# Kernel tuning notes

Hardware: AMD Instinct MI355X
Metric: run time of the kernel (lower is better)

Reference implementation:

```python
import jax, jax.numpy as jnp
import numpy as np

N_NODES = 100000
N_EDGES = 1600000
N_FEAT = 128
N_CLASSES = 10
N_GRAPHS = 256


def setup_inputs() -> dict:
    key = jax.random.key(0)
    ks = jax.random.split(key, 16)
    x = jax.random.normal(ks[0], (N_NODES, N_FEAT), dtype=jnp.float32)
    edge_index = jax.random.randint(ks[1], (2, N_EDGES), 0, N_NODES, dtype=jnp.int64)
    batch = jnp.sort(jax.random.randint(ks[2], (N_NODES,), 0, N_GRAPHS, dtype=jnp.int64))
    s = 0.1
    # GAT1: in=128 -> heads=8, out_per_head=8, concat -> 64
    W1 = jax.random.normal(ks[3], (N_FEAT, 64), dtype=jnp.float32) * s
    a_src1 = jax.random.normal(ks[4], (8, 8), dtype=jnp.float32) * s
    a_dst1 = jax.random.normal(ks[5], (8, 8), dtype=jnp.float32) * s
    b1 = jnp.zeros((64,), jnp.float32)
    # GAT2: in=64 -> heads=1, out=128
    W2 = jax.random.normal(ks[6], (64, 128), dtype=jnp.float32) * s
    a_src2 = jax.random.normal(ks[7], (1, 128), dtype=jnp.float32) * s
    a_dst2 = jax.random.normal(ks[8], (1, 128), dtype=jnp.float32) * s
    b2 = jnp.zeros((128,), jnp.float32)
    fc_w = jax.random.normal(ks[9], (128, N_CLASSES), dtype=jnp.float32) * s
    fc_b = jnp.zeros((N_CLASSES,), jnp.float32)
    return {"x": x, "edge_index": edge_index, "batch": batch,
            "W1": W1, "a_src1": a_src1, "a_dst1": a_dst1, "b1": b1,
            "W2": W2, "a_src2": a_src2, "a_dst2": a_dst2, "b2": b2,
            "fc_w": fc_w, "fc_b": fc_b}


def _segment_softmax(e, seg, n):
    # e: [E, H]; softmax over edges sharing the same destination node
    m = jax.ops.segment_max(e, seg, num_segments=n)
    m = jnp.where(jnp.isfinite(m), m, jnp.zeros_like(m))  # guard isolated nodes
    ex = jnp.exp(e - m[seg])
    s = jax.ops.segment_sum(ex, seg, num_segments=n)
    return ex / (s[seg] + jnp.asarray(1e-16, e.dtype))


def _gat_conv(x, src, dst, W, a_src, a_dst, bias):
    # PyG GATConv (eval mode, self-loops already appended to src/dst)
    H, C = a_src.shape
    n = x.shape[0]
    h = (x @ W).reshape(n, H, C)                      # [N,H,C]
    al_s = jnp.einsum('nhc,hc->nh', h, a_src)          # [N,H]
    al_d = jnp.einsum('nhc,hc->nh', h, a_dst)
    e = jax.nn.leaky_relu(al_s[src] + al_d[dst], 0.2)  # [E,H]
    alpha = _segment_softmax(e, dst, n)                # [E,H]
    out = jax.ops.segment_sum(h[src] * alpha[..., None], dst, num_segments=n)  # [N,H,C]
    return out.reshape(n, H * C) + bias                # concat=True (H=1 layer2 is identity reshape)


def reference(x, edge_index, batch, W1, a_src1, a_dst1, b1, W2, a_src2, a_dst2, b2, fc_w, fc_b):
    n = x.shape[0]
    loop = jnp.arange(n, dtype=edge_index.dtype)
    src = jnp.concatenate([edge_index[0], loop])       # add self-loops (PyG default)
    dst = jnp.concatenate([edge_index[1], loop])
    x1 = jax.nn.relu(_gat_conv(x, src, dst, W1, a_src1, a_dst1, b1))
    # dropout p=0.6 is identity in eval mode
    x2 = _gat_conv(x1, src, dst, W2, a_src2, a_dst2, b2)
    cnt = jax.ops.segment_sum(jnp.ones((n,), x2.dtype), batch, num_segments=N_GRAPHS)
    pooled = jax.ops.segment_sum(x2, batch, num_segments=N_GRAPHS) / jnp.maximum(cnt, 1.0)[:, None]
    logits = pooled @ fc_w + fc_b
    return jax.nn.log_softmax(logits, axis=1)
```

## Files before the change

### kernel.cpp

```cpp
#include <hip/hip_runtime.h>
#include <math.h>

typedef unsigned int uint;
typedef unsigned short ushort;
typedef unsigned char uchar;
typedef __attribute__((ext_vector_type(2))) float v2f;

#define S1 4.0f
#define S2 16.0f

template <bool HI>
__device__ inline v2f fp8x2f(uint u) {
    return __builtin_amdgcn_cvt_pk_f32_fp8((int)u, HI);
}

__global__ __launch_bounds__(256) void k_gemm1(const float* __restrict__ x,
                                               const float* __restrict__ W1,
                                               const float* __restrict__ as1,
                                               const float* __restrict__ ad1,
                                               uchar* __restrict__ h1f8,
                                               float* __restrict__ al1s,
                                               float* __restrict__ al1d, int N) {
    __shared__ float sB[128 * 64];
    __shared__ float sA[64 * 68];
    const int t = threadIdx.x;
    const int n0 = blockIdx.x * 64;
    {
        const float4* w4 = (const float4*)W1;
        float4* s4 = (float4*)sB;
#pragma unroll
        for (int i = 0; i < 8; ++i) s4[t + i * 256] = w4[t + i * 256];
    }
    const int r0 = (t >> 3) * 2;
    const int c0 = (t & 7) * 8;
    float acc0[8] = {0, 0, 0, 0, 0, 0, 0, 0};
    float acc1[8] = {0, 0, 0, 0, 0, 0, 0, 0};
    for (int kb = 0; kb < 2; ++kb) {
        __syncthreads();
#pragma unroll
        for (int i = 0; i < 4; ++i) {
            int idx = t + i * 256;
            int r = idx >> 4, kc = idx & 15;
            int n = n0 + r;
            float4 v = make_float4(0.f, 0.f, 0.f, 0.f);
            if (n < N) v = ((const float4*)x)[(size_t)n * 32 + kb * 16 + kc];
            *(float4*)&sA[r * 68 + kc * 4] = v;
        }
        __syncthreads();
        const float* bptr = &sB[kb * 64 * 64];
#pragma unroll 8
        for (int kk = 0; kk < 64; ++kk) {
            float a0 = sA[r0 * 68 + kk];
            float a1 = sA[(r0 + 1) * 68 + kk];
            const float* bp = &bptr[kk * 64 + c0];
            float4 b0 = *(const float4*)bp;
            float4 b1v = *(const float4*)(bp + 4);
            acc0[0] += a0 * b0.x; acc0[1] += a0 * b0.y; acc0[2] += a0 * b0.z; acc0[3] += a0 * b0.w;
            acc0[4] += a0 * b1v.x; acc0[5] += a0 * b1v.y; acc0[6] += a0 * b1v.z; acc0[7] += a0 * b1v.w;
            acc1[0] += a1 * b0.x; acc1[1] += a1 * b0.y; acc1[2] += a1 * b0.z; acc1[3] += a1 * b0.w;
            acc1[4] += a1 * b1v.x; acc1[5] += a1 * b1v.y; acc1[6] += a1 * b1v.z; acc1[7] += a1 * b1v.w;
        }
    }
    float ps0 = 0.f, pd0 = 0.f, ps1 = 0.f, pd1 = 0.f;
#pragma unroll
    for (int i = 0; i < 8; ++i) {
        float ws = as1[c0 + i], wd = ad1[c0 + i];
        ps0 += acc0[i] * ws; pd0 += acc0[i] * wd;
        ps1 += acc1[i] * ws; pd1 += acc1[i] * wd;
    }
    int n = n0 + r0;
    int head = t & 7;
    if (n < N) {
        int q0 = 0, q1 = 0;
        q0 = __builtin_amdgcn_cvt_pk_fp8_f32(acc0[0] * S1, acc0[1] * S1, q0, false);
        q0 = __builtin_amdgcn_cvt_pk_fp8_f32(acc0[2] * S1, acc0[3] * S1, q0, true);
        q1 = __builtin_amdgcn_cvt_pk_fp8_f32(acc0[4] * S1, acc0[5] * S1, q1, false);
        q1 = __builtin_amdgcn_cvt_pk_fp8_f32(acc0[6] * S1, acc0[7] * S1, q1, true);
        uint2 p; p.x = (uint)q0; p.y = (uint)q1;
        *(uint2*)&h1f8[(size_t)n * 64 + c0] = p;
        al1s[(size_t)n * 8 + head] = ps0;
        al1d[(size_t)n * 8 + head] = pd0;
    }
    if (n + 1 < N) {
        int q0 = 0, q1 = 0;
        q0 = __builtin_amdgcn_cvt_pk_fp8_f32(acc1[0] * S1, acc1[1] * S1, q0, false);
        q0 = __builtin_amdgcn_cvt_pk_fp8_f32(acc1[2] * S1, acc1[3] * S1, q0, true);
        q1 = __builtin_amdgcn_cvt_pk_fp8_f32(acc1[4] * S1, acc1[5] * S1, q1, false);
        q1 = __builtin_amdgcn_cvt_pk_fp8_f32(acc1[6] * S1, acc1[7] * S1, q1, true);
        uint2 p; p.x = (uint)q0; p.y = (uint)q1;
        *(uint2*)&h1f8[(size_t)(n + 1) * 64 + c0] = p;
        al1s[(size_t)(n + 1) * 8 + head] = ps1;
        al1d[(size_t)(n + 1) * 8 + head] = pd1;
    }
}

__global__ __launch_bounds__(256) void k_gemm2(const float* __restrict__ x1pre,
                                               const float* __restrict__ W2,
                                               const float* __restrict__ b1,
                                               const float* __restrict__ as2,
                                               const float* __restrict__ ad2,
                                               uchar* __restrict__ h2f8,
                                               float* __restrict__ al2s,
                                               float* __restrict__ al2d, int N) {
    __shared__ float sB[64 * 128];
    __shared__ float sA[64 * 68];
    const int t = threadIdx.x;
    const int n0 = blockIdx.x * 64;
    {
        const float4* w4 = (const float4*)W2;
        float4* s4 = (float4*)sB;
#pragma unroll
        for (int i = 0; i < 8; ++i) s4[t + i * 256] = w4[t + i * 256];
    }
#pragma unroll
    for (int i = 0; i < 4; ++i) {
        int idx = t + i * 256;
        int r = idx >> 4, kc = idx & 15;
        int n = n0 + r;
        float4 v = make_float4(0.f, 0.f, 0.f, 0.f);
        if (n < N) {
            v = ((const float4*)x1pre)[(size_t)n * 16 + kc];
            float4 bb = ((const float4*)b1)[kc];
            v.x = fmaxf(v.x + bb.x, 0.f);
            v.y = fmaxf(v.y + bb.y, 0.f);
            v.z = fmaxf(v.z + bb.z, 0.f);
            v.w = fmaxf(v.w + bb.w, 0.f);
        }
        *(float4*)&sA[r * 68 + kc * 4] = v;
    }
    __syncthreads();
    const int r0 = (t >> 3) * 2;
    const int cb = (t & 7) * 4;
    float acc0[16], acc1[16];
#pragma unroll
    for (int i = 0; i < 16; ++i) { acc0[i] = 0.f; acc1[i] = 0.f; }
#pragma unroll 4
    for (int k = 0; k < 64; ++k) {
        float a0 = sA[r0 * 68 + k];
        float a1 = sA[(r0 + 1) * 68 + k];
#pragma unroll
        for (int j = 0; j < 4; ++j) {
            float4 b = *(const float4*)&sB[k * 128 + cb + 32 * j];
            acc0[j * 4 + 0] += a0 * b.x; acc0[j * 4 + 1] += a0 * b.y;
            acc0[j * 4 + 2] += a0 * b.z; acc0[j * 4 + 3] += a0 * b.w;
            acc1[j * 4 + 0] += a1 * b.x; acc1[j * 4 + 1] += a1 * b.y;
            acc1[j * 4 + 2] += a1 * b.z; acc1[j * 4 + 3] += a1 * b.w;
        }
    }
    float ps0 = 0.f, pd0 = 0.f, ps1 = 0.f, pd1 = 0.f;
#pragma unroll
    for (int j = 0; j < 4; ++j)
#pragma unroll
        for (int i = 0; i < 4; ++i) {
            int cc = cb + 32 * j + i;
            float ws = as2[cc], wd = ad2[cc];
            ps0 += acc0[j * 4 + i] * ws; pd0 += acc0[j * 4 + i] * wd;
            ps1 += acc1[j * 4 + i] * ws; pd1 += acc1[j * 4 + i] * wd;
        }
#pragma unroll
    for (int off = 1; off < 8; off <<= 1) {
        ps0 += __shfl_xor(ps0, off); pd0 += __shfl_xor(pd0, off);
        ps1 += __shfl_xor(ps1, off); pd1 += __shfl_xor(pd1, off);
    }
    int n = n0 + r0;
    if (n < N) {
#pragma unroll
        for (int j = 0; j < 4; ++j) {
            int q = 0;
            q = __builtin_amdgcn_cvt_pk_fp8_f32(acc0[j * 4 + 0] * S2, acc0[j * 4 + 1] * S2, q, false);
            q = __builtin_amdgcn_cvt_pk_fp8_f32(acc0[j * 4 + 2] * S2, acc0[j * 4 + 3] * S2, q, true);
            *(uint*)&h2f8[(size_t)n * 128 + cb + 32 * j] = (uint)q;
        }
        if ((t & 7) == 0) { al2s[n] = ps0; al2d[n] = pd0; }
    }
    if (n + 1 < N) {
#pragma unroll
        for (int j = 0; j < 4; ++j) {
            int q = 0;
            q = __builtin_amdgcn_cvt_pk_fp8_f32(acc1[j * 4 + 0] * S2, acc1[j * 4 + 1] * S2, q, false);
            q = __builtin_amdgcn_cvt_pk_fp8_f32(acc1[j * 4 + 2] * S2, acc1[j * 4 + 3] * S2, q, true);
            *(uint*)&h2f8[(size_t)(n + 1) * 128 + cb + 32 * j] = (uint)q;
        }
        if ((t & 7) == 0) { al2s[n + 1] = ps1; al2d[n + 1] = pd1; }
    }
}


__global__ __launch_bounds__(256) void k_hist(const int* __restrict__ dst,
                                              int* __restrict__ counts,
                                              int E, int CH, int NB) {
    __shared__ int hist[784];
    int t = threadIdx.x, b = blockIdx.x;
    for (int k = t; k < NB; k += 256) hist[k] = 0;
    __syncthreads();
    int e0 = b * CH;
    int e1 = e0 + CH; if (e1 > E) e1 = E;
    for (int e = e0 + t; e < e1; e += 256)
        atomicAdd(&hist[dst[e] >> 7], 1);
    __syncthreads();
    for (int k = t; k < NB; k += 256) counts[(size_t)b * NB + k] = hist[k];
}

__global__ __launch_bounds__(256) void k_bscan(int* __restrict__ counts,
                                               int* __restrict__ btot,
                                               int C, int NB) {
    __shared__ int sh[256];
    int t = threadIdx.x, k = blockIdx.x;
    int v[4];
#pragma unroll
    for (int i = 0; i < 4; ++i) {
        int b = t * 4 + i;
        v[i] = (b < C) ? counts[(size_t)b * NB + k] : 0;
    }
    int s = v[0] + v[1] + v[2] + v[3];
    sh[t] = s;
    __syncthreads();
    int accv = s;
    for (int off = 1; off < 256; off <<= 1) {
        int u = (t >= off) ? sh[t - off] : 0;
        __syncthreads();
        accv += u;
        sh[t] = accv;
        __syncthreads();
    }
    int excl = accv - s;
#pragma unroll
    for (int i = 0; i < 4; ++i) {
        int b = t * 4 + i;
        if (b < C) counts[(size_t)b * NB + k] = excl;
        excl += v[i];
    }
    if (t == 255) btot[k] = accv;
}

__global__ void k_bscan2(const int* __restrict__ btot, int* __restrict__ bbase,
                         int NB, int E) {
    __shared__ int sh[1024];
    int t = threadIdx.x;
    int v = (t < NB) ? btot[t] : 0;
    sh[t] = v;
    __syncthreads();
    int accv = v;
    for (int off = 1; off < 1024; off <<= 1) {
        int u = (t >= off) ? sh[t - off] : 0;
        __syncthreads();
        accv += u;
        sh[t] = accv;
        __syncthreads();
    }
    if (t < NB) bbase[t] = accv - v;
    if (t == 0) bbase[NB] = E;
}

__global__ __launch_bounds__(256) void k_bucket(const int* __restrict__ src,
                                                const int* __restrict__ dst,
                                                const int* __restrict__ counts,
                                                const int* __restrict__ bbase,
                                                int* __restrict__ ebuf,
                                                int E, int CH, int NB) {
    __shared__ int pos[784];
    int t = threadIdx.x, b = blockIdx.x;
    for (int k = t; k < NB; k += 256)
        pos[k] = bbase[k] + counts[(size_t)b * NB + k];
    __syncthreads();
    int e0 = b * CH;
    int e1 = e0 + CH; if (e1 > E) e1 = E;
    for (int e = e0 + t; e < e1; e += 256) {
        int d = dst[e], s = src[e];
        int p = atomicAdd(&pos[d >> 7], 1);
        ebuf[p] = (int)((uint)s | ((uint)(d & 127) << 25));
    }
}

__global__ __launch_bounds__(256) void k_csr(const int* __restrict__ bbase,
                                             const int* __restrict__ ebuf,
                                             int* __restrict__ row_ptr,
                                             int* __restrict__ col,
                                             int N, int E) {
    __shared__ int cnt[128];
    __shared__ int fill[128];
    __shared__ int rowb[128];
    __shared__ int sh[256];
    int t = threadIdx.x, k = blockIdx.x;
    int lo = bbase[k], hi = bbase[k + 1];
    int nlo = k << 7;
    int nn = N - nlo; if (nn > 128) nn = 128;
    if (t < 128) { cnt[t] = 0; fill[t] = 0; }
    __syncthreads();
    for (int i = lo + t; i < hi; i += 256)
        atomicAdd(&cnt[((uint)ebuf[i]) >> 25], 1);
    __syncthreads();
    int v = (t < nn) ? (cnt[t] + 1) : 0;
    sh[t] = v;
    __syncthreads();
    int accv = v;
    for (int off = 1; off < 256; off <<= 1) {
        int u = (t >= off) ? sh[t - off] : 0;
        __syncthreads();
        accv += u;
        sh[t] = accv;
        __syncthreads();
    }
    int fbase = lo + nlo;
    if (t < nn) {
        int rb = fbase + accv - v;
        rowb[t] = rb;
        row_ptr[nlo + t] = rb;
        col[rb + cnt[t]] = nlo + t;
    }
    if (k == 0 && t == 0) row_ptr[N] = E + N;
    __syncthreads();
    for (int i = lo + t; i < hi; i += 256) {
        uint e = (uint)ebuf[i];
        int j = (int)(e >> 25);
        int r = atomicAdd(&fill[j], 1);
        col[rowb[j] + r] = (int)(e & 0x1FFFFFFu);
    }
}

__global__ __launch_bounds__(256) void k_edge1(const uchar* __restrict__ h1f8,
                                               const float* __restrict__ al1s,
                                               const float* __restrict__ al1d,
                                               const int* __restrict__ row_ptr,
                                               const int* __restrict__ col,
                                               float* __restrict__ x1pre, int N) {
    int node = blockIdx.x * 4 + (threadIdx.x >> 6);
    if (node >= N) return;
    const int lane = threadIdx.x & 63;
    const int e8 = lane >> 3;
    const int h = lane & 7;
    const int g = lane >> 4;
    const int k4 = lane & 15;
    const int hh = k4 >> 1;
    const uint co = (uint)(k4 * 4);
    float a_d = al1d[(((uint)node) << 3) | (uint)h];
    const int s0 = row_ptr[node], s1 = row_ptr[node + 1];
    float den_part = 0.f;
    v2f accL = {0.f, 0.f};
    v2f accH = {0.f, 0.f};
    for (int base = s0; base < s1; base += 64) {
        int idx = base + lane;
        int cidx = idx < s1 ? idx : s1 - 1;
        int my_col = col[cidx];
        int cnt = s1 - base; if (cnt > 64) cnt = 64;
        int cntR = (cnt + 3) & ~3;
        int i = 0;
        for (; i + 16 <= cntR; i += 16) {
            int cA = __shfl(my_col, i + g);
            int cB = __shfl(my_col, i + 4 + g);
            int cC = __shfl(my_col, i + 8 + g);
            int cD = __shfl(my_col, i + 12 + g);
            uint hA = *(const uint*)(h1f8 + ((((uint)cA) << 6) | co));
            uint hB = *(const uint*)(h1f8 + ((((uint)cB) << 6) | co));
            uint hC = *(const uint*)(h1f8 + ((((uint)cC) << 6) | co));
            uint hD = *(const uint*)(h1f8 + ((((uint)cD) << 6) | co));
            int c0 = __shfl(my_col, i + e8);
            int c1 = __shfl(my_col, i + 8 + e8);
            float e0v = *(al1s + ((((uint)c0) << 3) | (uint)h)) + a_d;
            float e1v = *(al1s + ((((uint)c1) << 3) | (uint)h)) + a_d;
            e0v = e0v > 0.f ? e0v : 0.2f * e0v;
            e1v = e1v > 0.f ? e1v : 0.2f * e1v;
            float w0 = (base + i + e8 < s1) ? __expf(e0v) : 0.f;
            float w1 = (base + i + 8 + e8 < s1) ? __expf(e1v) : 0.f;
            den_part += w0 + w1;
            float wA = __shfl(w0, g * 8 + hh);
            float wB = __shfl(w0, (4 + g) * 8 + hh);
            float wC = __shfl(w1, g * 8 + hh);
            float wD = __shfl(w1, (4 + g) * 8 + hh);
            v2f wA2 = {wA, wA}, wB2 = {wB, wB}, wC2 = {wC, wC}, wD2 = {wD, wD};
            accL += wA2 * fp8x2f<false>(hA);
            accH += wA2 * fp8x2f<true>(hA);
            accL += wB2 * fp8x2f<false>(hB);
            accH += wB2 * fp8x2f<true>(hB);
            accL += wC2 * fp8x2f<false>(hC);
            accH += wC2 * fp8x2f<true>(hC);
            accL += wD2 * fp8x2f<false>(hD);
            accH += wD2 * fp8x2f<true>(hD);
        }
        int rem = cntR - i;
        if (rem & 8) {
            int cA = __shfl(my_col, i + g);
            int cB = __shfl(my_col, i + 4 + g);
            uint hA = *(const uint*)(h1f8 + ((((uint)cA) << 6) | co));
            uint hB = *(const uint*)(h1f8 + ((((uint)cB) << 6) | co));
            int c0 = __shfl(my_col, i + e8);
            float e0v = *(al1s + ((((uint)c0) << 3) | (uint)h)) + a_d;
            e0v = e0v > 0.f ? e0v : 0.2f * e0v;
            float w0 = (base + i + e8 < s1) ? __expf(e0v) : 0.f;
            den_part += w0;
            float wA = __shfl(w0, g * 8 + hh);
            float wB = __shfl(w0, (4 + g) * 8 + hh);
            v2f wA2 = {wA, wA}, wB2 = {wB, wB};
            accL += wA2 * fp8x2f<false>(hA);
            accH += wA2 * fp8x2f<true>(hA);
            accL += wB2 * fp8x2f<false>(hB);
            accH += wB2 * fp8x2f<true>(hB);
            i += 8;
        }
        if (rem & 4) {
            int cA = __shfl(my_col, i + g);
            uint hA = *(const uint*)(h1f8 + ((((uint)cA) << 6) | co));
            int c0 = __shfl(my_col, i + e8);
            float e0v = *(al1s + ((((uint)c0) << 3) | (uint)h)) + a_d;
            e0v = e0v > 0.f ? e0v : 0.2f * e0v;
            float w0 = (base + i + e8 < s1) ? __expf(e0v) : 0.f;
            den_part += w0;
            float wA = __shfl(w0, g * 8 + hh);
            v2f wA2 = {wA, wA};
            accL += wA2 * fp8x2f<false>(hA);
            accH += wA2 * fp8x2f<true>(hA);
        }
    }
    float a0 = accL.x, a1 = accL.y, a2 = accH.x, a3 = accH.y;
    a0 += __shfl_xor(a0, 16); a0 += __shfl_xor(a0, 32);
    a1 += __shfl_xor(a1, 16); a1 += __shfl_xor(a1, 32);
    a2 += __shfl_xor(a2, 16); a2 += __shfl_xor(a2, 32);
    a3 += __shfl_xor(a3, 16); a3 += __shfl_xor(a3, 32);
    den_part += __shfl_xor(den_part, 8);
    den_part += __shfl_xor(den_part, 16);
    den_part += __shfl_xor(den_part, 32);
    float den = __shfl(den_part, hh);
    if (lane < 16) {
        float invd = 1.f / (den * S1);
        ((float4*)x1pre)[(size_t)node * 16 + k4] =
            make_float4(a0 * invd, a1 * invd, a2 * invd, a3 * invd);
    }
}

__global__ __launch_bounds__(256) void k_edge2(const uchar* __restrict__ h2f8,
                                               const float* __restrict__ al2s,
                                               const float* __restrict__ al2d,
                                               const int* __restrict__ row_ptr,
                                               const int* __restrict__ col,
                                               const float* __restrict__ b2,
                                               float* __restrict__ x2, int N) {
    int node = blockIdx.x * 4 + (threadIdx.x >> 6);
    if (node >= N) return;
    const int lane = threadIdx.x & 63;
    const int g = lane >> 4;
    const int k8 = lane & 15;
    const uint co = (uint)(k8 * 8);
    float a_d = al2d[node];
    int s0 = row_ptr[node], s1 = row_ptr[node + 1];
    v2f acc0 = {0.f, 0.f}, acc1 = {0.f, 0.f}, acc2 = {0.f, 0.f}, acc3 = {0.f, 0.f};
    float den = 0.f;
    for (int base = s0; base < s1; base += 64) {
        int idx = base + lane;
        int cidx = idx < s1 ? idx : s1 - 1;
        int my_col = col[cidx];
        float my_e = *(al2s + (uint)my_col) + a_d;
        my_e = my_e > 0.f ? my_e : 0.2f * my_e;
        float my_w = (idx < s1) ? __expf(my_e) : 0.f;
        den += my_w;
        int cnt = s1 - base; if (cnt > 64) cnt = 64;
        int cntR = (cnt + 3) & ~3;
        int i = 0;
        for (; i + 16 <= cntR; i += 16) {
            int eA = i + g, eB = i + 4 + g, eC = i + 8 + g, eD = i + 12 + g;
            int cA = __shfl(my_col, eA), cB = __shfl(my_col, eB);
            int cC = __shfl(my_col, eC), cD = __shfl(my_col, eD);
            float wA = __shfl(my_w, eA), wB = __shfl(my_w, eB);
            float wC = __shfl(my_w, eC), wD = __shfl(my_w, eD);
            uint2 hA = *(const uint2*)(h2f8 + ((((uint)cA) << 7) | co));
            uint2 hB = *(const uint2*)(h2f8 + ((((uint)cB) << 7) | co));
            uint2 hC = *(const uint2*)(h2f8 + ((((uint)cC) << 7) | co));
            uint2 hD = *(const uint2*)(h2f8 + ((((uint)cD) << 7) | co));
            v2f wA2 = {wA, wA}, wB2 = {wB, wB}, wC2 = {wC, wC}, wD2 = {wD, wD};
            acc0 += wA2 * fp8x2f<false>(hA.x);
            acc1 += wA2 * fp8x2f<true>(hA.x);
            acc2 += wA2 * fp8x2f<false>(hA.y);
            acc3 += wA2 * fp8x2f<true>(hA.y);
            acc0 += wB2 * fp8x2f<false>(hB.x);
            acc1 += wB2 * fp8x2f<true>(hB.x);
            acc2 += wB2 * fp8x2f<false>(hB.y);
            acc3 += wB2 * fp8x2f<true>(hB.y);
            acc0 += wC2 * fp8x2f<false>(hC.x);
            acc1 += wC2 * fp8x2f<true>(hC.x);
            acc2 += wC2 * fp8x2f<false>(hC.y);
            acc3 += wC2 * fp8x2f<true>(hC.y);
            acc0 += wD2 * fp8x2f<false>(hD.x);
            acc1 += wD2 * fp8x2f<true>(hD.x);
            acc2 += wD2 * fp8x2f<false>(hD.y);
            acc3 += wD2 * fp8x2f<true>(hD.y);
        }
        int rem = cntR - i;
        if (rem & 8) {
            int eA = i + g, eB = i + 4 + g;
            int cA = __shfl(my_col, eA), cB = __shfl(my_col, eB);
            float wA = __shfl(my_w, eA), wB = __shfl(my_w, eB);
            uint2 hA = *(const uint2*)(h2f8 + ((((uint)cA) << 7) | co));
            uint2 hB = *(const uint2*)(h2f8 + ((((uint)cB) << 7) | co));
            v2f wA2 = {wA, wA}, wB2 = {wB, wB};
            acc0 += wA2 * fp8x2f<false>(hA.x);
            acc1 += wA2 * fp8x2f<true>(hA.x);
            acc2 += wA2 * fp8x2f<false>(hA.y);
            acc3 += wA2 * fp8x2f<true>(hA.y);
            acc0 += wB2 * fp8x2f<false>(hB.x);
            acc1 += wB2 * fp8x2f<true>(hB.x);
            acc2 += wB2 * fp8x2f<false>(hB.y);
            acc3 += wB2 * fp8x2f<true>(hB.y);
            i += 8;
        }
        if (rem & 4) {
            int eA = i + g;
            int cA = __shfl(my_col, eA);
            float wA = __shfl(my_w, eA);
            uint2 hA = *(const uint2*)(h2f8 + ((((uint)cA) << 7) | co));
            v2f wA2 = {wA, wA};
            acc0 += wA2 * fp8x2f<false>(hA.x);
            acc1 += wA2 * fp8x2f<true>(hA.x);
            acc2 += wA2 * fp8x2f<false>(hA.y);
            acc3 += wA2 * fp8x2f<true>(hA.y);
        }
    }
#pragma unroll
    for (int off = 1; off < 64; off <<= 1) den += __shfl_xor(den, off);
    float r0 = acc0.x, r1 = acc0.y, r2 = acc1.x, r3 = acc1.y;
    float r4 = acc2.x, r5 = acc2.y, r6 = acc3.x, r7 = acc3.y;
    r0 += __shfl_xor(r0, 16); r0 += __shfl_xor(r0, 32);
    r1 += __shfl_xor(r1, 16); r1 += __shfl_xor(r1, 32);
    r2 += __shfl_xor(r2, 16); r2 += __shfl_xor(r2, 32);
    r3 += __shfl_xor(r3, 16); r3 += __shfl_xor(r3, 32);
    r4 += __shfl_xor(r4, 16); r4 += __shfl_xor(r4, 32);
    r5 += __shfl_xor(r5, 16); r5 += __shfl_xor(r5, 32);
    r6 += __shfl_xor(r6, 16); r6 += __shfl_xor(r6, 32);
    r7 += __shfl_xor(r7, 16); r7 += __shfl_xor(r7, 32);
    if (lane < 16) {
        float invd = 1.f / (den * S2);
        const float4* bb = (const float4*)b2;
        float4 o0 = bb[k8 * 2], o1 = bb[k8 * 2 + 1];
        float4* dst = (float4*)(x2 + (size_t)node * 128 + k8 * 8);
        dst[0] = make_float4(r0 * invd + o0.x, r1 * invd + o0.y,
                             r2 * invd + o0.z, r3 * invd + o0.w);
        dst[1] = make_float4(r4 * invd + o1.x, r5 * invd + o1.y,
                             r6 * invd + o1.z, r7 * invd + o1.w);
    }
}

__global__ __launch_bounds__(128) void k_pool(const float* __restrict__ x2,
                                              const int* __restrict__ batch,
                                              float* __restrict__ pooled,
                                              float* __restrict__ cnt, int N) {
    int t = threadIdx.x;
    int nstart = blockIdx.x * 128;
    if (nstart >= N) return;
    int nend = nstart + 128;
    if (nend > N) nend = N;
    float acc = 0.f;
    int cur = batch[nstart];
    int count = 0;
    for (int n = nstart; n < nend; ++n) {
        int g = batch[n];
        if (g != cur) {
            atomicAdd(&pooled[(size_t)cur * 128 + t], acc);
            if (t == 0) atomicAdd(&cnt[cur], (float)count);
            acc = 0.f;
            count = 0;
            cur = g;
        }
        acc += x2[(size_t)n * 128 + t];
        ++count;
    }
    atomicAdd(&pooled[(size_t)cur * 128 + t], acc);
    if (t == 0) atomicAdd(&cnt[cur], (float)count);
}

__global__ __launch_bounds__(64) void k_fc(const float* __restrict__ pooled,
                                           const float* __restrict__ cnt,
                                           const float* __restrict__ fcw,
                                           const float* __restrict__ fcb,
                                           float* __restrict__ out, int G) {
    int g = blockIdx.x;
    int c = threadIdx.x;
    float2 p = ((const float2*)pooled)[(size_t)g * 64 + c];
    float inv = 1.f / fmaxf(cnt[g], 1.f);
    p.x *= inv; p.y *= inv;
    float l[10];
#pragma unroll
    for (int j = 0; j < 10; ++j)
        l[j] = p.x * fcw[(2 * c) * 10 + j] + p.y * fcw[(2 * c + 1) * 10 + j];
#pragma unroll
    for (int j = 0; j < 10; ++j)
        for (int off = 1; off < 64; off <<= 1) l[j] += __shfl_xor(l[j], off);
    if (c == 0) {
        float lj[10];
        float m = -1e30f;
#pragma unroll
        for (int j = 0; j < 10; ++j) {
            lj[j] = l[j] + fcb[j];
            m = fmaxf(m, lj[j]);
        }
        float s = 0.f;
#pragma unroll
        for (int j = 0; j < 10; ++j) s += expf(lj[j] - m);
        float ls = logf(s);
#pragma unroll
        for (int j = 0; j < 10; ++j) out[(size_t)g * 10 + j] = lj[j] - m - ls;
    }
}

extern "C" void kernel_launch(void* const* d_in, const int* in_sizes, int n_in,
                              void* d_out, int out_size, void* d_ws, size_t ws_size,
                              hipStream_t stream) {
    const float* x     = (const float*)d_in[0];
    const int*   ei    = (const int*)d_in[1];
    const int*   batch = (const int*)d_in[2];
    const float* W1    = (const float*)d_in[3];
    const float* as1   = (const float*)d_in[4];
    const float* ad1   = (const float*)d_in[5];
    const float* b1    = (const float*)d_in[6];
    const float* W2    = (const float*)d_in[7];
    const float* as2   = (const float*)d_in[8];
    const float* ad2   = (const float*)d_in[9];
    const float* b2    = (const float*)d_in[10];
    const float* fcw   = (const float*)d_in[11];
    const float* fcb   = (const float*)d_in[12];
    float* out = (float*)d_out;

    const int N = in_sizes[0] / 128;
    const int E = in_sizes[1] / 2;
    const int G = out_size / 10;
    const int* srcp = ei;
    const int* dstp = ei + E;

    float* wf = (float*)d_ws;
    uchar* h1f8   = (uchar*)wf;
    float* x1pre  = wf + (size_t)N * 16;
    float* x2     = wf;
    uchar* h2f8   = (uchar*)(wf + (size_t)N * 128);
    float* al1s_  = wf + (size_t)N * 160;
    float* al1d_  = wf + (size_t)N * 168;
    float* al2s_  = wf + (size_t)N * 176;
    float* al2d_  = wf + (size_t)N * 177;
    float* pooled = wf + (size_t)N * 178;
    float* cnt    = pooled + (size_t)G * 128;

    const int NB = (N + 127) >> 7;
    const int C  = 1024;
    const int CH = (E + C - 1) / C;

    int* ib = (int*)(((uintptr_t)(cnt + G) + 15) & ~(uintptr_t)15);
    int* ebuf    = ib;
    int* counts  = ib + (size_t)E;
    int* btot    = counts + (size_t)C * NB;
    int* bbase   = btot + NB;
    int* row_ptr = bbase + NB + 1;
    int* col     = row_ptr + N + 1;

    size_t zbytes = ((size_t)G * 128 + G) * sizeof(float);
    (void)hipMemsetAsync(pooled, 0, zbytes, stream);

    const int nb64 = (N + 63) / 64;
    const int nb4  = (N + 3) / 4;
    const int nbP  = (N + 127) / 128;

    k_hist<<<C, 256, 0, stream>>>(dstp, counts, E, CH, NB);
    k_gemm1<<<nb64, 256, 0, stream>>>(x, W1, as1, ad1, h1f8, al1s_, al1d_, N);
    k_bscan<<<NB, 256, 0, stream>>>(counts, btot, C, NB);
    k_bscan2<<<1, 1024, 0, stream>>>(btot, bbase, NB, E);
    k_bucket<<<C, 256, 0, stream>>>(srcp, dstp, counts, bbase, ebuf, E, CH, NB);
    k_csr<<<NB, 256, 0, stream>>>(bbase, ebuf, row_ptr, col, N, E);
    k_edge1<<<nb4, 256, 0, stream>>>(h1f8, al1s_, al1d_, row_ptr, col, x1pre, N);
    k_gemm2<<<nb64, 256, 0, stream>>>(x1pre, W2, b1, as2, ad2, h2f8, al2s_, al2d_, N);
    k_edge2<<<nb4, 256, 0, stream>>>(h2f8, al2s_, al2d_, row_ptr, col, b2, x2, N);
    k_pool<<<nbP, 128, 0, stream>>>(x2, batch, pooled, cnt, N);
    k_fc<<<G, 64, 0, stream>>>(pooled, cnt, fcw, fcb, out, G);
}
```

Baseline: 360.3 us.

## Fuse mean-pooling into edge2 and compute attention weights per lane directly

Edge kernels stop staging column indices and softmax weights through wave shuffles. Each lane now loads col and the source attention logit directly and computes its own exp weight, so the denominator reduction is shorter. Edge2 no longer writes x2; it atomically adds its normalized output into the per-graph pooled buffer, the pool kernel is removed, and bias b2 is applied in k_fc. This trades the x2 write/read round trip and one launch for many float atomics onto 256 graph rows, plus redundant exp and logit gathers per lane.

Result: slower. 1.015 ms (+181.8%).

```diff
diff --git a/kernel.cpp b/kernel.cpp
--- a/kernel.cpp
+++ b/kernel.cpp
@@ -327,46 +327,40 @@
     int node = blockIdx.x * 4 + (threadIdx.x >> 6);
     if (node >= N) return;
     const int lane = threadIdx.x & 63;
-    const int e8 = lane >> 3;
-    const int h = lane & 7;
     const int g = lane >> 4;
     const int k4 = lane & 15;
     const int hh = k4 >> 1;
     const uint co = (uint)(k4 * 4);
-    float a_d = al1d[(((uint)node) << 3) | (uint)h];
+    const float a_dh = al1d[(((uint)node) << 3) | (uint)hh];
     const int s0 = row_ptr[node], s1 = row_ptr[node + 1];
     float den_part = 0.f;
     v2f accL = {0.f, 0.f};
     v2f accH = {0.f, 0.f};
     for (int base = s0; base < s1; base += 64) {
-        int idx = base + lane;
-        int cidx = idx < s1 ? idx : s1 - 1;
-        int my_col = col[cidx];
         int cnt = s1 - base; if (cnt > 64) cnt = 64;
         int cntR = (cnt + 3) & ~3;
         int i = 0;
         for (; i + 16 <= cntR; i += 16) {
-            int cA = __shfl(my_col, i + g);
-            int cB = __shfl(my_col, i + 4 + g);
-            int cC = __shfl(my_col, i + 8 + g);
-            int cD = __shfl(my_col, i + 12 + g);
+            int eA = base + i + g, eB = eA + 4, eC = eA + 8, eD = eA + 12;
+            int xD = eD < s1 ? eD : s1 - 1;
+            int cA = col[eA], cB = col[eB], cC = col[eC], cD = col[xD];
             uint hA = *(const uint*)(h1f8 + ((((uint)cA) << 6) | co));
             uint hB = *(const uint*)(h1f8 + ((((uint)cB) << 6) | co));
             uint hC = *(const uint*)(h1f8 + ((((uint)cC) << 6) | co));
             uint hD = *(const uint*)(h1f8 + ((((uint)cD) << 6) | co));
-            int c0 = __shfl(my_col, i + e8);
-            int c1 = __shfl(my_col, i + 8 + e8);
-            float e0v = *(al1s + ((((uint)c0) << 3) | (uint)h)) + a_d;
-            float e1v = *(al1s + ((((uint)c1) << 3) | (uint)h)) + a_d;
-            e0v = e0v > 0.f ? e0v : 0.2f * e0v;
-            e1v = e1v > 0.f ? e1v : 0.2f * e1v;
-            float w0 = (base + i + e8 < s1) ? __expf(e0v) : 0.f;
-            float w1 = (base + i + 8 + e8 < s1) ? __expf(e1v) : 0.f;
-            den_part += w0 + w1;
-            float wA = __shfl(w0, g * 8 + hh);
-            float wB = __shfl(w0, (4 + g) * 8 + hh);
-            float wC = __shfl(w1, g * 8 + hh);
-            float wD = __shfl(w1, (4 + g) * 8 + hh);
+            float lA = al1s[((((uint)cA) << 3) | (uint)hh)] + a_dh;
+            float lB = al1s[((((uint)cB) << 3) | (uint)hh)] + a_dh;
+            float lC = al1s[((((uint)cC) << 3) | (uint)hh)] + a_dh;
+            float lD = al1s[((((uint)cD) << 3) | (uint)hh)] + a_dh;
+            lA = lA > 0.f ? lA : 0.2f * lA;
+            lB = lB > 0.f ? lB : 0.2f * lB;
+            lC = lC > 0.f ? lC : 0.2f * lC;
+            lD = lD > 0.f ? lD : 0.2f * lD;
+            float wA = __expf(lA);
+            float wB = __expf(lB);
+            float wC = __expf(lC);
+            float wD = (eD < s1) ? __expf(lD) : 0.f;
+            den_part += wA + wB + wC + wD;
             v2f wA2 = {wA, wA}, wB2 = {wB, wB}, wC2 = {wC, wC}, wD2 = {wD, wD};
             accL += wA2 * fp8x2f<false>(hA);
             accH += wA2 * fp8x2f<true>(hA);
@@ -379,17 +373,18 @@
         }
         int rem = cntR - i;
         if (rem & 8) {
-            int cA = __shfl(my_col, i + g);
-            int cB = __shfl(my_col, i + 4 + g);
+            int eA = base + i + g, eB = eA + 4;
+            int xB = eB < s1 ? eB : s1 - 1;
+            int cA = col[eA], cB = col[xB];
             uint hA = *(const uint*)(h1f8 + ((((uint)cA) << 6) | co));
             uint hB = *(const uint*)(h1f8 + ((((uint)cB) << 6) | co));
-            int c0 = __shfl(my_col, i + e8);
-            float e0v = *(al1s + ((((uint)c0) << 3) | (uint)h)) + a_d;
-            e0v = e0v > 0.f ? e0v : 0.2f * e0v;
-            float w0 = (base + i + e8 < s1) ? __expf(e0v) : 0.f;
-            den_part += w0;
-            float wA = __shfl(w0, g * 8 + hh);
-            float wB = __shfl(w0, (4 + g) * 8 + hh);
+            float lA = al1s[((((uint)cA) << 3) | (uint)hh)] + a_dh;
+            float lB = al1s[((((uint)cB) << 3) | (uint)hh)] + a_dh;
+            lA = lA > 0.f ? lA : 0.2f * lA;
+            lB = lB > 0.f ? lB : 0.2f * lB;
+            float wA = __expf(lA);
+            float wB = (eB < s1) ? __expf(lB) : 0.f;
+            den_part += wA + wB;
             v2f wA2 = {wA, wA}, wB2 = {wB, wB};
             accL += wA2 * fp8x2f<false>(hA);
             accH += wA2 * fp8x2f<true>(hA);
@@ -398,14 +393,14 @@
             i += 8;
         }
         if (rem & 4) {
-            int cA = __shfl(my_col, i + g);
+            int eA = base + i + g;
+            int xA = eA < s1 ? eA : s1 - 1;
+            int cA = col[xA];
             uint hA = *(const uint*)(h1f8 + ((((uint)cA) << 6) | co));
-            int c0 = __shfl(my_col, i + e8);
-            float e0v = *(al1s + ((((uint)c0) << 3) | (uint)h)) + a_d;
-            e0v = e0v > 0.f ? e0v : 0.2f * e0v;
-            float w0 = (base + i + e8 < s1) ? __expf(e0v) : 0.f;
-            den_part += w0;
-            float wA = __shfl(w0, g * 8 + hh);
+            float lA = al1s[((((uint)cA) << 3) | (uint)hh)] + a_dh;
+            lA = lA > 0.f ? lA : 0.2f * lA;
+            float wA = (eA < s1) ? __expf(lA) : 0.f;
+            den_part += wA;
             v2f wA2 = {wA, wA};
             accL += wA2 * fp8x2f<false>(hA);
             accH += wA2 * fp8x2f<true>(hA);
@@ -416,12 +411,10 @@
     a1 += __shfl_xor(a1, 16); a1 += __shfl_xor(a1, 32);
     a2 += __shfl_xor(a2, 16); a2 += __shfl_xor(a2, 32);
     a3 += __shfl_xor(a3, 16); a3 += __shfl_xor(a3, 32);
-    den_part += __shfl_xor(den_part, 8);
     den_part += __shfl_xor(den_part, 16);
     den_part += __shfl_xor(den_part, 32);
-    float den = __shfl(den_part, hh);
     if (lane < 16) {
-        float invd = 1.f / (den * S1);
+        float invd = 1.f / (den_part * S1);
         ((float4*)x1pre)[(size_t)node * 16 + k4] =
             make_float4(a0 * invd, a1 * invd, a2 * invd, a3 * invd);
     }
@@ -432,39 +425,45 @@
                                                const float* __restrict__ al2d,
                                                const int* __restrict__ row_ptr,
                                                const int* __restrict__ col,
-                                               const float* __restrict__ b2,
-                                               float* __restrict__ x2, int N) {
+                                               const int* __restrict__ batchv,
+                                               float* __restrict__ pooled,
+                                               float* __restrict__ cntg, int N) {
     int node = blockIdx.x * 4 + (threadIdx.x >> 6);
     if (node >= N) return;
     const int lane = threadIdx.x & 63;
     const int g = lane >> 4;
     const int k8 = lane & 15;
     const uint co = (uint)(k8 * 8);
-    float a_d = al2d[node];
-    int s0 = row_ptr[node], s1 = row_ptr[node + 1];
+    const int gg = batchv[node];
+    const float a_d = al2d[node];
+    const int s0 = row_ptr[node], s1 = row_ptr[node + 1];
     v2f acc0 = {0.f, 0.f}, acc1 = {0.f, 0.f}, acc2 = {0.f, 0.f}, acc3 = {0.f, 0.f};
-    float den = 0.f;
+    float den_part = 0.f;
     for (int base = s0; base < s1; base += 64) {
-        int idx = base + lane;
-        int cidx = idx < s1 ? idx : s1 - 1;
-        int my_col = col[cidx];
-        float my_e = *(al2s + (uint)my_col) + a_d;
-        my_e = my_e > 0.f ? my_e : 0.2f * my_e;
-        float my_w = (idx < s1) ? __expf(my_e) : 0.f;
-        den += my_w;
         int cnt = s1 - base; if (cnt > 64) cnt = 64;
         int cntR = (cnt + 3) & ~3;
         int i = 0;
         for (; i + 16 <= cntR; i += 16) {
-            int eA = i + g, eB = i + 4 + g, eC = i + 8 + g, eD = i + 12 + g;
-            int cA = __shfl(my_col, eA), cB = __shfl(my_col, eB);
-            int cC = __shfl(my_col, eC), cD = __shfl(my_col, eD);
-            float wA = __shfl(my_w, eA), wB = __shfl(my_w, eB);
-            float wC = __shfl(my_w, eC), wD = __shfl(my_w, eD);
+            int eA = base + i + g, eB = eA + 4, eC = eA + 8, eD = eA + 12;
+            int xD = eD < s1 ? eD : s1 - 1;
+            int cA = col[eA], cB = col[eB], cC = col[eC], cD = col[xD];
             uint2 hA = *(const uint2*)(h2f8 + ((((uint)cA) << 7) | co));
             uint2 hB = *(const uint2*)(h2f8 + ((((uint)cB) << 7) | co));
             uint2 hC = *(const uint2*)(h2f8 + ((((uint)cC) << 7) | co));
             uint2 hD = *(const uint2*)(h2f8 + ((((uint)cD) << 7) | co));
+            float lA = al2s[(uint)cA] + a_d;
+            float lB = al2s[(uint)cB] + a_d;
+            float lC = al2s[(uint)cC] + a_d;
+            float lD = al2s[(uint)cD] + a_d;
+            lA = lA > 0.f ? lA : 0.2f * lA;
+            lB = lB > 0.f ? lB : 0.2f * lB;
+            lC = lC > 0.f ? lC : 0.2f * lC;
+            lD = lD > 0.f ? lD : 0.2f * lD;
+            float wA = __expf(lA);
+            float wB = __expf(lB);
+            float wC = __expf(lC);
+            float wD = (eD < s1) ? __expf(lD) : 0.f;
+            den_part += wA + wB + wC + wD;
             v2f wA2 = {wA, wA}, wB2 = {wB, wB}, wC2 = {wC, wC}, wD2 = {wD, wD};
             acc0 += wA2 * fp8x2f<false>(hA.x);
             acc1 += wA2 * fp8x2f<true>(hA.x);
@@ -485,11 +484,18 @@
         }
         int rem = cntR - i;
         if (rem & 8) {
-            int eA = i + g, eB = i + 4 + g;
-            int cA = __shfl(my_col, eA), cB = __shfl(my_col, eB);
-            float wA = __shfl(my_w, eA), wB = __shfl(my_w, eB);
+            int eA = base + i + g, eB = eA + 4;
+            int xB = eB < s1 ? eB : s1 - 1;
+            int cA = col[eA], cB = col[xB];
             uint2 hA = *(const uint2*)(h2f8 + ((((uint)cA) << 7) | co));
             uint2 hB = *(const uint2*)(h2f8 + ((((uint)cB) << 7) | co));
+            float lA = al2s[(uint)cA] + a_d;
+            float lB = al2s[(uint)cB] + a_d;
+            lA = lA > 0.f ? lA : 0.2f * lA;
+            lB = lB > 0.f ? lB : 0.2f * lB;
+            float wA = __expf(lA);
+            float wB = (eB < s1) ? __expf(lB) : 0.f;
+            den_part += wA + wB;
             v2f wA2 = {wA, wA}, wB2 = {wB, wB};
             acc0 += wA2 * fp8x2f<false>(hA.x);
             acc1 += wA2 * fp8x2f<true>(hA.x);
@@ -502,10 +508,14 @@
             i += 8;
         }
         if (rem & 4) {
-            int eA = i + g;
-            int cA = __shfl(my_col, eA);
-            float wA = __shfl(my_w, eA);
+            int eA = base + i + g;
+            int xA = eA < s1 ? eA : s1 - 1;
+            int cA = col[xA];
             uint2 hA = *(const uint2*)(h2f8 + ((((uint)cA) << 7) | co));
+            float lA = al2s[(uint)cA] + a_d;
+            lA = lA > 0.f ? lA : 0.2f * lA;
+            float wA = (eA < s1) ? __expf(lA) : 0.f;
+            den_part += wA;
             v2f wA2 = {wA, wA};
             acc0 += wA2 * fp8x2f<false>(hA.x);
             acc1 += wA2 * fp8x2f<true>(hA.x);
@@ -513,8 +523,8 @@
             acc3 += wA2 * fp8x2f<true>(hA.y);
         }
     }
-#pragma unroll
-    for (int off = 1; off < 64; off <<= 1) den += __shfl_xor(den, off);
+    den_part += __shfl_xor(den_part, 16);
+    den_part += __shfl_xor(den_part, 32);
     float r0 = acc0.x, r1 = acc0.y, r2 = acc1.x, r3 = acc1.y;
     float r4 = acc2.x, r5 = acc2.y, r6 = acc3.x, r7 = acc3.y;
     r0 += __shfl_xor(r0, 16); r0 += __shfl_xor(r0, 32);
@@ -526,55 +536,33 @@
     r6 += __shfl_xor(r6, 16); r6 += __shfl_xor(r6, 32);
     r7 += __shfl_xor(r7, 16); r7 += __shfl_xor(r7, 32);
     if (lane < 16) {
-        float invd = 1.f / (den * S2);
-        const float4* bb = (const float4*)b2;
-        float4 o0 = bb[k8 * 2], o1 = bb[k8 * 2 + 1];
-        float4* dst = (float4*)(x2 + (size_t)node * 128 + k8 * 8);
-        dst[0] = make_float4(r0 * invd + o0.x, r1 * invd + o0.y,
-                             r2 * invd + o0.z, r3 * invd + o0.w);
-        dst[1] = make_float4(r4 * invd + o1.x, r5 * invd + o1.y,
-                             r6 * invd + o1.z, r7 * invd + o1.w);
-    }
-}
-
-__global__ __launch_bounds__(128) void k_pool(const float* __restrict__ x2,
-                                              const int* __restrict__ batch,
-                                              float* __restrict__ pooled,
-                                              float* __restrict__ cnt, int N) {
-    int t = threadIdx.x;
-    int nstart = blockIdx.x * 128;
-    if (nstart >= N) return;
-    int nend = nstart + 128;
-    if (nend > N) nend = N;
-    float acc = 0.f;
-    int cur = batch[nstart];
-    int count = 0;
-    for (int n = nstart; n < nend; ++n) {
-        int g = batch[n];
-        if (g != cur) {
-            atomicAdd(&pooled[(size_t)cur * 128 + t], acc);
-            if (t == 0) atomicAdd(&cnt[cur], (float)count);
-            acc = 0.f;
-            count = 0;
-            cur = g;
-        }
-        acc += x2[(size_t)n * 128 + t];
-        ++count;
-    }
-    atomicAdd(&pooled[(size_t)cur * 128 + t], acc);
-    if (t == 0) atomicAdd(&cnt[cur], (float)count);
+        float invd = 1.f / (den_part * S2);
+        float* pr = pooled + (size_t)gg * 128 + co;
+        atomicAdd(&pr[0], r0 * invd);
+        atomicAdd(&pr[1], r1 * invd);
+        atomicAdd(&pr[2], r2 * invd);
+        atomicAdd(&pr[3], r3 * invd);
+        atomicAdd(&pr[4], r4 * invd);
+        atomicAdd(&pr[5], r5 * invd);
+        atomicAdd(&pr[6], r6 * invd);
+        atomicAdd(&pr[7], r7 * invd);
+    }
+    if (lane == 0) atomicAdd(&cntg[gg], 1.0f);
 }
 
 __global__ __launch_bounds__(64) void k_fc(const float* __restrict__ pooled,
                                            const float* __restrict__ cnt,
+                                           const float* __restrict__ b2,
                                            const float* __restrict__ fcw,
                                            const float* __restrict__ fcb,
                                            float* __restrict__ out, int G) {
     int g = blockIdx.x;
     int c = threadIdx.x;
     float2 p = ((const float2*)pooled)[(size_t)g * 64 + c];
+    float2 bb = ((const float2*)b2)[c];
     float inv = 1.f / fmaxf(cnt[g], 1.f);
-    p.x *= inv; p.y *= inv;
+    p.x = p.x * inv + bb.x;
+    p.y = p.y * inv + bb.y;
     float l[10];
 #pragma unroll
     for (int j = 0; j < 10; ++j)
@@ -626,7 +614,6 @@
     float* wf = (float*)d_ws;
     uchar* h1f8   = (uchar*)wf;
     float* x1pre  = wf + (size_t)N * 16;
-    float* x2     = wf;
     uchar* h2f8   = (uchar*)(wf + (size_t)N * 128);
     float* al1s_  = wf + (size_t)N * 160;
     float* al1d_  = wf + (size_t)N * 168;
@@ -652,7 +639,6 @@
 
     const int nb64 = (N + 63) / 64;
     const int nb4  = (N + 3) / 4;
-    const int nbP  = (N + 127) / 128;
 
     k_hist<<<C, 256, 0, stream>>>(dstp, counts, E, CH, NB);
     k_gemm1<<<nb64, 256, 0, stream>>>(x, W1, as1, ad1, h1f8, al1s_, al1d_, N);
@@ -662,7 +648,6 @@
     k_csr<<<NB, 256, 0, stream>>>(bbase, ebuf, row_ptr, col, N, E);
     k_edge1<<<nb4, 256, 0, stream>>>(h1f8, al1s_, al1d_, row_ptr, col, x1pre, N);
     k_gemm2<<<nb64, 256, 0, stream>>>(x1pre, W2, b1, as2, ad2, h2f8, al2s_, al2d_, N);
-    k_edge2<<<nb4, 256, 0, stream>>>(h2f8, al2s_, al2d_, row_ptr, col, b2, x2, N);
-    k_pool<<<nbP, 128, 0, stream>>>(x2, batch, pooled, cnt, N);
-    k_fc<<<G, 64, 0, stream>>>(pooled, cnt, fcw, fcb, out, G);
-}
+    k_edge2<<<nb4, 256, 0, stream>>>(h2f8, al2s_, al2d_, row_ptr, col, batch, pooled, cnt, N);
+    k_fc<<<G, 64, 0, stream>>>(pooled, cnt, b2, fcw, fcb, out, G);
+}
```
